# Optimization experiments

Measured on AMD Instinct MI355X. Metric: run time of the kernel, lower is better.

Reference implementation:

```python
import jax, jax.numpy as jnp
import numpy as np

ALPHA = 0.2  # LeakyReLU negative slope

def setup_inputs() -> dict:
    key = jax.random.key(0)
    kx, kw, kb, ka = jax.random.split(key, 4)
    B, K, D, H = 4, 256, 128, 4
    x = jax.random.normal(kx, (B, K, D), dtype=jnp.float32)
    # Per-head Linear(2D -> D): stored as (H, 2D, D), i.e. transposed torch layout (y = v @ W + b)
    W = jax.random.normal(kw, (H, 2 * D, D), dtype=jnp.float32) * (1.0 / np.sqrt(2 * D))
    lin_b = jax.random.normal(kb, (H, D), dtype=jnp.float32) * 0.01
    # Per-head attention vector a: (H, D)
    a = jax.random.normal(ka, (H, D), dtype=jnp.float32) * (1.0 / np.sqrt(D))
    # Per-head additive bias over attention logits, initialized to zeros like the torch module
    bias = jnp.zeros((H, K, K), dtype=jnp.float32)
    return {"x": x, "W": W, "lin_b": lin_b, "a": a, "bias": bias}

def reference(x, W, lin_b, a, bias):
    # GATv2, dense all-pairs attention over K nodes, eval mode (dropout off).
    # Faithful decomposition: Linear(concat(x_i, x_j)) == x_i @ W_src + x_j @ W_dst + b
    B, K, D = x.shape
    H = W.shape[0]
    outs = []
    for h in range(H):  # small fixed head count; each head has distinct params
        W_src, W_dst = W[h, :D], W[h, D:]          # (D, D) each
        left = x @ W_src                            # (B, K, D) -> contribution of node i
        right = x @ W_dst                           # (B, K, D) -> contribution of node j
        s = left[:, :, None, :] + right[:, None, :, :] + lin_b[h]  # (B, K, K, D)
        s = jnp.where(s > 0, s, ALPHA * s)          # LeakyReLU
        e = jnp.einsum('bijd,d->bij', s, a[h]) + bias[h]           # (B, K, K)
        attn = jax.nn.softmax(e, axis=2)
        outs.append(attn @ x)                       # (B, K, D)
    return jnp.mean(jnp.stack(outs, axis=-1), axis=-1)
```

## Files before the change

### kernel.cpp

```cpp
#include <hip/hip_runtime.h>
#include <math.h>

constexpr int Kc = 256, Dc = 128, Mc = 1024;

typedef _Float16 h2_t __attribute__((ext_vector_type(2)));
union U32H2 { unsigned int u; h2_t h; };
__device__ inline h2_t u2h(unsigned int u) { U32H2 x; x.u = u; return x.h; }
__device__ inline unsigned int h2u(h2_t h) { U32H2 x; x.h = h; return x.u; }
__device__ inline unsigned int packh(float a, float b) {
    h2_t h; h.x = (_Float16)a; h.y = (_Float16)b; return h2u(h);
}

__device__ inline float estep(unsigned int r, unsigned int l, h2_t av, float acc) {
    h2_t s = u2h(r) + u2h(l);
    unsigned int t = h2u(s) & 0x7FFF7FFFu;
#if __has_builtin(__builtin_amdgcn_fdot2)
    return __builtin_amdgcn_fdot2(u2h(t), av, acc, false);
#else
    h2_t th = u2h(t);
    return fmaf((float)th.x, (float)av.x, fmaf((float)th.y, (float)av.y, acc));
#endif
}

__global__ __launch_bounds__(256) void k1(const float* __restrict__ x,
                                          const float* __restrict__ W,
                                          const float* __restrict__ lin_b,
                                          const float* __restrict__ a,
                                          unsigned int* __restrict__ Lpp,
                                          unsigned int* __restrict__ Rtp,
                                          float* __restrict__ eb) {
    __shared__ float As[128][32];
    __shared__ float Bs[128][64];
    __shared__ float red[4][16][4];

    const int tid = threadIdx.x;
    const int bid = blockIdx.x;
    const int tx = tid & 15, ty = tid >> 4;
    const bool isL = (bid < 256);

    int h, b, m0, n0, dt;
    if (isL) {
        const int nt = bid & 1, mt = (bid >> 1) & 31;
        h = (bid >> 6) & 3;
        m0 = mt * 32; n0 = nt * 64; b = 0; dt = 0;
        {
            const int m_l = tid & 31, kq = tid >> 5;
            #pragma unroll
            for (int c = 0; c < 4; ++c) {
                const int k0 = kq * 16 + c * 4;
                const float4 v = *(const float4*)&x[(m0 + m_l) * Dc + k0];
                As[k0 + 0][m_l] = v.x; As[k0 + 1][m_l] = v.y;
                As[k0 + 2][m_l] = v.z; As[k0 + 3][m_l] = v.w;
            }
        }
        {
            const int n_l = tid & 63, kq = tid >> 6;
            const float* Wb = W + (h * 2) * Dc * Dc;
            #pragma unroll
            for (int kk = 0; kk < 32; ++kk) {
                const int k = kq * 32 + kk;
                Bs[k][n_l] = Wb[k * Dc + n0 + n_l];
            }
        }
    } else {
        const int r_ = bid - 256;
        const int jt = r_ & 3;
        dt = (r_ >> 2) & 3;
        b  = (r_ >> 4) & 3;
        h  = (r_ >> 6) & 3;
        m0 = dt * 32;
        n0 = jt * 64;
        {
            const int d_l = tid & 31, kq = tid >> 5;
            const float* Wb = W + ((h * 2 + 1) * Dc) * Dc;
            #pragma unroll
            for (int kk = 0; kk < 16; ++kk) {
                const int k = kq * 16 + kk;
                As[k][d_l] = Wb[k * Dc + m0 + d_l];
            }
        }
        {
            const int j_l = tid & 63, kq = tid >> 6;
            #pragma unroll
            for (int c = 0; c < 8; ++c) {
                const int k0 = kq * 32 + c * 4;
                const float4 v = *(const float4*)&x[(b * Kc + n0 + j_l) * Dc + k0];
                Bs[k0 + 0][j_l] = v.x; Bs[k0 + 1][j_l] = v.y;
                Bs[k0 + 2][j_l] = v.z; Bs[k0 + 3][j_l] = v.w;
            }
        }
    }
    __syncthreads();

    float acc[2][4];
    #pragma unroll
    for (int r = 0; r < 2; ++r)
        #pragma unroll
        for (int c = 0; c < 4; ++c) acc[r][c] = 0.f;

    #pragma unroll 16
    for (int k = 0; k < 128; ++k) {
        const float2 xa = *(const float2*)&As[k][ty * 2];
        const float4 wb = *(const float4*)&Bs[k][tx * 4];
        acc[0][0] = fmaf(xa.x, wb.x, acc[0][0]);
        acc[0][1] = fmaf(xa.x, wb.y, acc[0][1]);
        acc[0][2] = fmaf(xa.x, wb.z, acc[0][2]);
        acc[0][3] = fmaf(xa.x, wb.w, acc[0][3]);
        acc[1][0] = fmaf(xa.y, wb.x, acc[1][0]);
        acc[1][1] = fmaf(xa.y, wb.y, acc[1][1]);
        acc[1][2] = fmaf(xa.y, wb.z, acc[1][2]);
        acc[1][3] = fmaf(xa.y, wb.w, acc[1][3]);
    }

    if (isL) {
        const float4 lv = *(const float4*)&lin_b[h * Dc + n0 + tx * 4];
        #pragma unroll
        for (int r = 0; r < 2; ++r) {
            uint2 pk;
            pk.x = packh(acc[r][0] + lv.x, acc[r][1] + lv.y);
            pk.y = packh(acc[r][2] + lv.z, acc[r][3] + lv.w);
            *(uint2*)&Lpp[(h * Mc + m0 + ty * 2 + r) * 64 + (n0 >> 1) + tx * 2] = pk;
        }
    } else {
        {
            uint4 pk;
            pk.x = packh(acc[0][0], acc[1][0]);
            pk.y = packh(acc[0][1], acc[1][1]);
            pk.z = packh(acc[0][2], acc[1][2]);
            pk.w = packh(acc[0][3], acc[1][3]);
            *(uint4*)&Rtp[((h * 4 + b) * 64 + (m0 >> 1) + ty) * Kc + n0 + tx * 4] = pk;
        }
        const float2 av = *(const float2*)&a[h * Dc + m0 + ty * 2];
        float p0 = 0.4f * (av.x * acc[0][0] + av.y * acc[1][0]);
        float p1 = 0.4f * (av.x * acc[0][1] + av.y * acc[1][1]);
        float p2 = 0.4f * (av.x * acc[0][2] + av.y * acc[1][2]);
        float p3 = 0.4f * (av.x * acc[0][3] + av.y * acc[1][3]);
        p0 += __shfl_xor(p0, 16, 64); p0 += __shfl_xor(p0, 32, 64);
        p1 += __shfl_xor(p1, 16, 64); p1 += __shfl_xor(p1, 32, 64);
        p2 += __shfl_xor(p2, 16, 64); p2 += __shfl_xor(p2, 32, 64);
        p3 += __shfl_xor(p3, 16, 64); p3 += __shfl_xor(p3, 32, 64);
        if (((tid >> 4) & 3) == 0) {
            const int w = tid >> 6;
            red[w][tx][0] = p0; red[w][tx][1] = p1;
            red[w][tx][2] = p2; red[w][tx][3] = p3;
        }
        __syncthreads();
        if (tid < 64) {
            const int txl = tid >> 2, c = tid & 3;
            const float v = red[0][txl][c] + red[1][txl][c] + red[2][txl][c] + red[3][txl][c];
            eb[((h * 4 + b) * 4 + dt) * Kc + n0 + tid] = 1.5f * v;
        }
    }
}

#define E4(ACC, LPV)                               \
    ACC.x = estep(rr.x, LPV, av, ACC.x);           \
    ACC.y = estep(rr.y, LPV, av, ACC.y);           \
    ACC.z = estep(rr.z, LPV, av, ACC.z);           \
    ACC.w = estep(rr.w, LPV, av, ACC.w);

__global__ __launch_bounds__(256) void k2(const float* __restrict__ x,
                                          const float* __restrict__ a,
                                          const float* __restrict__ bias,
                                          const unsigned int* __restrict__ Lpp,
                                          const unsigned int* __restrict__ Rtp,
                                          const float* __restrict__ eb,
                                          float* __restrict__ out) {
    __shared__ float red[256 * 12];
    __shared__ unsigned int lpT2[4 * 64 * 2];
    __shared__ unsigned int aa2s[4 * 64];
    __shared__ float plbar[2 * Kc];

    const int tid = threadIdx.x;
    const int L = blockIdx.x;
    const int xcd = L & 7;
    const int b = xcd >> 1;
    const int it = ((L >> 3) << 1) | (xcd & 1);
    const int i0 = it * 2;

    {
        const int h = tid >> 6, dp = tid & 63;
        uint2 v;
        v.x = Lpp[(h * Mc + b * Kc + i0 + 0) * 64 + dp];
        v.y = Lpp[(h * Mc + b * Kc + i0 + 1) * 64 + dp];
        *(uint2*)&lpT2[(h * 64 + dp) * 2] = v;
        aa2s[tid] = packh(0.4f * a[h * Dc + 2 * dp], 0.4f * a[h * Dc + 2 * dp + 1]);
    }
    if (tid < 128) ((float4*)plbar)[tid] = make_float4(0.f, 0.f, 0.f, 0.f);
    __syncthreads();

    const int dq = tid >> 6, j4 = tid & 63;
    const int w = tid >> 6, l = tid & 63;

    #pragma unroll 1
    for (int h = 0; h < 4; ++h) {
        const int hb = h * 4 + b;
        float4 acc0 = make_float4(0.f, 0.f, 0.f, 0.f);
        float4 acc1 = make_float4(0.f, 0.f, 0.f, 0.f);
        {
            const unsigned int* rb = Rtp + (hb * 64 + dq * 16) * Kc + j4 * 4;
            const unsigned int* lt = lpT2 + (h * 64 + dq * 16) * 2;
            const unsigned int* at = aa2s + h * 64 + dq * 16;
            #pragma unroll
            for (int dp = 0; dp < 16; ++dp) {
                const uint4 rr = *(const uint4*)(rb + dp * Kc);
                const uint2 lp2 = *(const uint2*)(lt + dp * 2);
                const h2_t av = u2h(at[dp]);
                E4(acc0, lp2.x);
                E4(acc1, lp2.y);
            }
        }
        {
            float* myred = red + tid * 12;
            *(float4*)&myred[0] = acc0;
            *(float4*)&myred[4] = acc1;
        }
        __syncthreads();

        if (w < 2) {
            float4 e0 = make_float4(0.f, 0.f, 0.f, 0.f);
            #pragma unroll
            for (int q4 = 0; q4 < 4; ++q4) {
                const float4 v = *(const float4*)&red[(q4 * 64 + l) * 12 + w * 4];
                e0.x += v.x; e0.y += v.y; e0.z += v.z; e0.w += v.w;
            }
            float4 ebs = make_float4(0.f, 0.f, 0.f, 0.f);
            #pragma unroll
            for (int seg = 0; seg < 4; ++seg) {
                const float4 v = *(const float4*)&eb[(hb * 4 + seg) * Kc + l * 4];
                ebs.x += v.x; ebs.y += v.y; ebs.z += v.z; ebs.w += v.w;
            }
            const float4 bv = *(const float4*)&bias[(h * Kc + i0 + w) * Kc + l * 4];
            e0.x += ebs.x + bv.x;
            e0.y += ebs.y + bv.y;
            e0.z += ebs.z + bv.z;
            e0.w += ebs.w + bv.w;

            float m = fmaxf(fmaxf(e0.x, e0.y), fmaxf(e0.z, e0.w));
            #pragma unroll
            for (int off = 1; off < 64; off <<= 1) m = fmaxf(m, __shfl_xor(m, off, 64));
            const float p0 = __expf(e0.x - m), p1 = __expf(e0.y - m);
            const float p2 = __expf(e0.z - m), p3 = __expf(e0.w - m);
            float s = p0 + p1 + p2 + p3;
            #pragma unroll
            for (int off = 1; off < 64; off <<= 1) s += __shfl_xor(s, off, 64);
            const float sc = 0.25f / s;
            float4 cur = *(float4*)&plbar[w * Kc + l * 4];
            cur.x = fmaf(p0, sc, cur.x);
            cur.y = fmaf(p1, sc, cur.y);
            cur.z = fmaf(p2, sc, cur.z);
            cur.w = fmaf(p3, sc, cur.w);
            *(float4*)&plbar[w * Kc + l * 4] = cur;
        }
        __syncthreads();
    }

    const int jq = tid >> 5, dd4 = tid & 31;
    float4 o0 = make_float4(0.f, 0.f, 0.f, 0.f);
    float4 o1 = make_float4(0.f, 0.f, 0.f, 0.f);
    {
        const float* xb = x + (b * Kc) * Dc + dd4 * 4;
        #pragma unroll 4
        for (int jj = 0; jj < 32; ++jj) {
            const int j = jj * 8 + jq;
            const float4 xv = *(const float4*)(xb + j * Dc);
            const float pv0 = plbar[j];
            const float pv1 = plbar[Kc + j];
            o0.x = fmaf(pv0, xv.x, o0.x); o0.y = fmaf(pv0, xv.y, o0.y);
            o0.z = fmaf(pv0, xv.z, o0.z); o0.w = fmaf(pv0, xv.w, o0.w);
            o1.x = fmaf(pv1, xv.x, o1.x); o1.y = fmaf(pv1, xv.y, o1.y);
            o1.z = fmaf(pv1, xv.z, o1.z); o1.w = fmaf(pv1, xv.w, o1.w);
        }
    }
    {
        float* myred = red + (jq * 32 + dd4) * 12;
        *(float4*)&myred[0] = o0;
        *(float4*)&myred[4] = o1;
    }
    __syncthreads();
    if (tid < 64) {
        const int i_f = tid >> 5, dd_f = tid & 31;
        float4 s = make_float4(0.f, 0.f, 0.f, 0.f);
        #pragma unroll
        for (int q = 0; q < 8; ++q) {
            const float4 v = *(const float4*)&red[(q * 32 + dd_f) * 12 + i_f * 4];
            s.x += v.x; s.y += v.y; s.z += v.z; s.w += v.w;
        }
        *(float4*)&out[(b * Kc + i0 + i_f) * Dc + dd_f * 4] = s;
    }
}

extern "C" void kernel_launch(void* const* d_in, const int* in_sizes, int n_in,
                              void* d_out, int out_size, void* d_ws, size_t ws_size,
                              hipStream_t stream) {
    const float* x     = (const float*)d_in[0];
    const float* W     = (const float*)d_in[1];
    const float* lin_b = (const float*)d_in[2];
    const float* a     = (const float*)d_in[3];
    const float* bias  = (const float*)d_in[4];
    float* out = (float*)d_out;

    unsigned int*   Lpp = (unsigned int*)d_ws;
    unsigned int*   Rtp = Lpp + 4 * Mc * 64;
    float*          eb  = (float*)(Rtp + 16 * 64 * Kc);

    k1<<<512, 256, 0, stream>>>(x, W, lin_b, a, Lpp, Rtp, eb);
    k2<<<512, 256, 0, stream>>>(x, a, bias, Lpp, Rtp, eb, out);
}
```

Baseline: 26.43 us.

## Use fp16 packed dot2 GEMM in k1 with larger 64x64 tiles

The projection GEMM in k1 now converts x and W to packed fp16 pairs in shared memory and accumulates with fdot2, halving LDS traffic and FMA instruction count. Tiles grow from 32x64 to 64x64 with a 4x4 register tile per thread, so the grid halves to 256 blocks, and the eb partial-sum segments drop from 4 to 2, with k2 updated to match. This lowers per-block overhead and instruction count but reduces parallelism on a large GPU and loses precision in the GEMM inputs.

```diff
diff --git a/kernel.cpp b/kernel.cpp
--- a/kernel.cpp
+++ b/kernel.cpp
@@ -10,6 +10,17 @@
 __device__ inline unsigned int packh(float a, float b) {
     h2_t h; h.x = (_Float16)a; h.y = (_Float16)b; return h2u(h);
 }
+
+#if __has_builtin(__builtin_amdgcn_fdot2)
+__device__ inline float dot2h(unsigned int a, unsigned int b, float c) {
+    return __builtin_amdgcn_fdot2(u2h(a), u2h(b), c, false);
+}
+#else
+__device__ inline float dot2h(unsigned int a, unsigned int b, float c) {
+    h2_t ah = u2h(a), bh = u2h(b);
+    return fmaf((float)ah.x, (float)bh.x, fmaf((float)ah.y, (float)bh.y, c));
+}
+#endif
 
 __device__ inline float estep(unsigned int r, unsigned int l, h2_t av, float acc) {
     h2_t s = u2h(r) + u2h(l);
@@ -29,112 +40,121 @@
                                           unsigned int* __restrict__ Lpp,
                                           unsigned int* __restrict__ Rtp,
                                           float* __restrict__ eb) {
-    __shared__ float As[128][32];
-    __shared__ float Bs[128][64];
+    __shared__ unsigned int As2[64 * 64];
+    __shared__ unsigned int Bs2[64 * 64];
     __shared__ float red[4][16][4];
 
     const int tid = threadIdx.x;
     const int bid = blockIdx.x;
     const int tx = tid & 15, ty = tid >> 4;
-    const bool isL = (bid < 256);
+    const bool isL = (bid < 128);
 
     int h, b, m0, n0, dt;
     if (isL) {
-        const int nt = bid & 1, mt = (bid >> 1) & 31;
-        h = (bid >> 6) & 3;
-        m0 = mt * 32; n0 = nt * 64; b = 0; dt = 0;
-        {
-            const int m_l = tid & 31, kq = tid >> 5;
-            #pragma unroll
-            for (int c = 0; c < 4; ++c) {
-                const int k0 = kq * 16 + c * 4;
-                const float4 v = *(const float4*)&x[(m0 + m_l) * Dc + k0];
-                As[k0 + 0][m_l] = v.x; As[k0 + 1][m_l] = v.y;
-                As[k0 + 2][m_l] = v.z; As[k0 + 3][m_l] = v.w;
+        const int nt = bid & 1, mt = (bid >> 1) & 15;
+        h = (bid >> 5) & 3; b = 0; dt = 0;
+        m0 = mt * 64; n0 = nt * 64;
+        {
+            const int m_l = tid & 63, kq = tid >> 6;
+            #pragma unroll
+            for (int c = 0; c < 8; ++c) {
+                const float4 v = *(const float4*)&x[(m0 + m_l) * Dc + kq * 32 + c * 4];
+                As2[(kq * 16 + c * 2 + 0) * 64 + m_l] = packh(v.x, v.y);
+                As2[(kq * 16 + c * 2 + 1) * 64 + m_l] = packh(v.z, v.w);
             }
         }
         {
             const int n_l = tid & 63, kq = tid >> 6;
             const float* Wb = W + (h * 2) * Dc * Dc;
             #pragma unroll
-            for (int kk = 0; kk < 32; ++kk) {
-                const int k = kq * 32 + kk;
-                Bs[k][n_l] = Wb[k * Dc + n0 + n_l];
+            for (int kk = 0; kk < 16; ++kk) {
+                const int k2 = kq * 16 + kk;
+                Bs2[k2 * 64 + n_l] =
+                    packh(Wb[(2 * k2) * Dc + n0 + n_l], Wb[(2 * k2 + 1) * Dc + n0 + n_l]);
             }
         }
     } else {
-        const int r_ = bid - 256;
+        const int r_ = bid - 128;
         const int jt = r_ & 3;
-        dt = (r_ >> 2) & 3;
-        b  = (r_ >> 4) & 3;
-        h  = (r_ >> 6) & 3;
-        m0 = dt * 32;
+        dt = (r_ >> 2) & 1;
+        b  = (r_ >> 3) & 3;
+        h  = (r_ >> 5) & 3;
+        m0 = dt * 64;
         n0 = jt * 64;
         {
-            const int d_l = tid & 31, kq = tid >> 5;
+            const int d_l = tid & 63, kq = tid >> 6;
             const float* Wb = W + ((h * 2 + 1) * Dc) * Dc;
             #pragma unroll
             for (int kk = 0; kk < 16; ++kk) {
-                const int k = kq * 16 + kk;
-                As[k][d_l] = Wb[k * Dc + m0 + d_l];
+                const int k2 = kq * 16 + kk;
+                As2[k2 * 64 + d_l] =
+                    packh(Wb[(2 * k2) * Dc + m0 + d_l], Wb[(2 * k2 + 1) * Dc + m0 + d_l]);
             }
         }
         {
             const int j_l = tid & 63, kq = tid >> 6;
             #pragma unroll
             for (int c = 0; c < 8; ++c) {
-                const int k0 = kq * 32 + c * 4;
-                const float4 v = *(const float4*)&x[(b * Kc + n0 + j_l) * Dc + k0];
-                Bs[k0 + 0][j_l] = v.x; Bs[k0 + 1][j_l] = v.y;
-                Bs[k0 + 2][j_l] = v.z; Bs[k0 + 3][j_l] = v.w;
+                const float4 v = *(const float4*)&x[(b * Kc + n0 + j_l) * Dc + kq * 32 + c * 4];
+                Bs2[(kq * 16 + c * 2 + 0) * 64 + j_l] = packh(v.x, v.y);
+                Bs2[(kq * 16 + c * 2 + 1) * 64 + j_l] = packh(v.z, v.w);
             }
         }
     }
     __syncthreads();
 
-    float acc[2][4];
+    float acc[4][4];
     #pragma unroll
-    for (int r = 0; r < 2; ++r)
+    for (int r = 0; r < 4; ++r)
         #pragma unroll
         for (int c = 0; c < 4; ++c) acc[r][c] = 0.f;
 
-    #pragma unroll 16
-    for (int k = 0; k < 128; ++k) {
-        const float2 xa = *(const float2*)&As[k][ty * 2];
-        const float4 wb = *(const float4*)&Bs[k][tx * 4];
-        acc[0][0] = fmaf(xa.x, wb.x, acc[0][0]);
-        acc[0][1] = fmaf(xa.x, wb.y, acc[0][1]);
-        acc[0][2] = fmaf(xa.x, wb.z, acc[0][2]);
-        acc[0][3] = fmaf(xa.x, wb.w, acc[0][3]);
-        acc[1][0] = fmaf(xa.y, wb.x, acc[1][0]);
-        acc[1][1] = fmaf(xa.y, wb.y, acc[1][1]);
-        acc[1][2] = fmaf(xa.y, wb.z, acc[1][2]);
-        acc[1][3] = fmaf(xa.y, wb.w, acc[1][3]);
+    #pragma unroll 8
+    for (int k2 = 0; k2 < 64; ++k2) {
+        const uint4 xa = *(const uint4*)&As2[k2 * 64 + ty * 4];
+        const uint4 wb = *(const uint4*)&Bs2[k2 * 64 + tx * 4];
+        acc[0][0] = dot2h(xa.x, wb.x, acc[0][0]);
+        acc[0][1] = dot2h(xa.x, wb.y, acc[0][1]);
+        acc[0][2] = dot2h(xa.x, wb.z, acc[0][2]);
+        acc[0][3] = dot2h(xa.x, wb.w, acc[0][3]);
+        acc[1][0] = dot2h(xa.y, wb.x, acc[1][0]);
+        acc[1][1] = dot2h(xa.y, wb.y, acc[1][1]);
+        acc[1][2] = dot2h(xa.y, wb.z, acc[1][2]);
+        acc[1][3] = dot2h(xa.y, wb.w, acc[1][3]);
+        acc[2][0] = dot2h(xa.z, wb.x, acc[2][0]);
+        acc[2][1] = dot2h(xa.z, wb.y, acc[2][1]);
+        acc[2][2] = dot2h(xa.z, wb.z, acc[2][2]);
+        acc[2][3] = dot2h(xa.z, wb.w, acc[2][3]);
+        acc[3][0] = dot2h(xa.w, wb.x, acc[3][0]);
+        acc[3][1] = dot2h(xa.w, wb.y, acc[3][1]);
+        acc[3][2] = dot2h(xa.w, wb.z, acc[3][2]);
+        acc[3][3] = dot2h(xa.w, wb.w, acc[3][3]);
     }
 
     if (isL) {
         const float4 lv = *(const float4*)&lin_b[h * Dc + n0 + tx * 4];
         #pragma unroll
-        for (int r = 0; r < 2; ++r) {
+        for (int r = 0; r < 4; ++r) {
             uint2 pk;
             pk.x = packh(acc[r][0] + lv.x, acc[r][1] + lv.y);
             pk.y = packh(acc[r][2] + lv.z, acc[r][3] + lv.w);
-            *(uint2*)&Lpp[(h * Mc + m0 + ty * 2 + r) * 64 + (n0 >> 1) + tx * 2] = pk;
+            *(uint2*)&Lpp[(h * Mc + m0 + ty * 4 + r) * 64 + (n0 >> 1) + tx * 2] = pk;
         }
     } else {
-        {
+        #pragma unroll
+        for (int rp = 0; rp < 2; ++rp) {
             uint4 pk;
-            pk.x = packh(acc[0][0], acc[1][0]);
-            pk.y = packh(acc[0][1], acc[1][1]);
-            pk.z = packh(acc[0][2], acc[1][2]);
-            pk.w = packh(acc[0][3], acc[1][3]);
-            *(uint4*)&Rtp[((h * 4 + b) * 64 + (m0 >> 1) + ty) * Kc + n0 + tx * 4] = pk;
-        }
-        const float2 av = *(const float2*)&a[h * Dc + m0 + ty * 2];
-        float p0 = 0.4f * (av.x * acc[0][0] + av.y * acc[1][0]);
-        float p1 = 0.4f * (av.x * acc[0][1] + av.y * acc[1][1]);
-        float p2 = 0.4f * (av.x * acc[0][2] + av.y * acc[1][2]);
-        float p3 = 0.4f * (av.x * acc[0][3] + av.y * acc[1][3]);
+            pk.x = packh(acc[2 * rp][0], acc[2 * rp + 1][0]);
+            pk.y = packh(acc[2 * rp][1], acc[2 * rp + 1][1]);
+            pk.z = packh(acc[2 * rp][2], acc[2 * rp + 1][2]);
+            pk.w = packh(acc[2 * rp][3], acc[2 * rp + 1][3]);
+            *(uint4*)&Rtp[((h * 4 + b) * 64 + (m0 >> 1) + ty * 2 + rp) * Kc + n0 + tx * 4] = pk;
+        }
+        const float4 av = *(const float4*)&a[h * Dc + m0 + ty * 4];
+        float p0 = 0.4f * (av.x * acc[0][0] + av.y * acc[1][0] + av.z * acc[2][0] + av.w * acc[3][0]);
+        float p1 = 0.4f * (av.x * acc[0][1] + av.y * acc[1][1] + av.z * acc[2][1] + av.w * acc[3][1]);
+        float p2 = 0.4f * (av.x * acc[0][2] + av.y * acc[1][2] + av.z * acc[2][2] + av.w * acc[3][2]);
+        float p3 = 0.4f * (av.x * acc[0][3] + av.y * acc[1][3] + av.z * acc[2][3] + av.w * acc[3][3]);
         p0 += __shfl_xor(p0, 16, 64); p0 += __shfl_xor(p0, 32, 64);
         p1 += __shfl_xor(p1, 16, 64); p1 += __shfl_xor(p1, 32, 64);
         p2 += __shfl_xor(p2, 16, 64); p2 += __shfl_xor(p2, 32, 64);
@@ -148,7 +168,7 @@
         if (tid < 64) {
             const int txl = tid >> 2, c = tid & 3;
             const float v = red[0][txl][c] + red[1][txl][c] + red[2][txl][c] + red[3][txl][c];
-            eb[((h * 4 + b) * 4 + dt) * Kc + n0 + tid] = 1.5f * v;
+            eb[((h * 4 + b) * 2 + dt) * Kc + n0 + tid] = 1.5f * v;
         }
     }
 }
@@ -224,11 +244,12 @@
                 const float4 v = *(const float4*)&red[(q4 * 64 + l) * 12 + w * 4];
                 e0.x += v.x; e0.y += v.y; e0.z += v.z; e0.w += v.w;
             }
-            float4 ebs = make_float4(0.f, 0.f, 0.f, 0.f);
-            #pragma unroll
-            for (int seg = 0; seg < 4; ++seg) {
-                const float4 v = *(const float4*)&eb[(hb * 4 + seg) * Kc + l * 4];
-                ebs.x += v.x; ebs.y += v.y; ebs.z += v.z; ebs.w += v.w;
+            float4 ebs;
+            {
+                const float4 v0 = *(const float4*)&eb[(hb * 2 + 0) * Kc + l * 4];
+                const float4 v1 = *(const float4*)&eb[(hb * 2 + 1) * Kc + l * 4];
+                ebs.x = v0.x + v1.x; ebs.y = v0.y + v1.y;
+                ebs.z = v0.z + v1.z; ebs.w = v0.w + v1.w;
             }
             const float4 bv = *(const float4*)&bias[(h * Kc + i0 + w) * Kc + l * 4];
             e0.x += ebs.x + bv.x;
@@ -304,6 +325,6 @@
     unsigned int*   Rtp = Lpp + 4 * Mc * 64;
     float*          eb  = (float*)(Rtp + 16 * 64 * Kc);
 
-    k1<<<512, 256, 0, stream>>>(x, W, lin_b, a, Lpp, Rtp, eb);
+    k1<<<256, 256, 0, stream>>>(x, W, lin_b, a, Lpp, Rtp, eb);
     k2<<<512, 256, 0, stream>>>(x, a, bias, Lpp, Rtp, eb, out);
 }
```

Result: faster. 25.19 us (-4.7%).
